# Kernel optimization log

Hardware: AMD Instinct MI355X
Metric: run time of the kernel (lower is better)

The kernel has to match this reference:

```python
import jax, jax.numpy as jnp
import numpy as np

VOCAB = 100000
EMBED = 64
HIDDEN = 256
SEQ = 200
BATCH = 4096


def setup_inputs() -> dict:
    key = jax.random.key(0)
    ks = jax.random.split(key, 12)
    s = 0.02
    return {
        "user_hist": jax.random.randint(ks[0], (BATCH, SEQ), 0, VOCAB),
        "target_item": jax.random.randint(ks[1], (BATCH,), 0, VOCAB),
        "user_emb": jax.random.normal(ks[2], (VOCAB, EMBED), jnp.float32) * s,
        "item_emb": jax.random.normal(ks[3], (VOCAB, EMBED), jnp.float32) * s,
        "attn_w1": jax.random.normal(ks[4], (4 * EMBED, HIDDEN), jnp.float32) * s,
        "attn_b1": jnp.zeros((HIDDEN,), jnp.float32),
        "attn_w2": jax.random.normal(ks[5], (HIDDEN, 1), jnp.float32) * s,
        "attn_b2": jnp.zeros((1,), jnp.float32),
        "mlp_w1": jax.random.normal(ks[6], (2 * EMBED, HIDDEN), jnp.float32) * s,
        "mlp_b1": jnp.zeros((HIDDEN,), jnp.float32),
        "mlp_w2": jax.random.normal(ks[7], (HIDDEN, 1), jnp.float32) * s,
        "mlp_b2": jnp.zeros((1,), jnp.float32),
    }


def reference(user_hist, target_item, user_emb, item_emb,
              attn_w1, attn_b1, attn_w2, attn_b2,
              mlp_w1, mlp_b1, mlp_w2, mlp_b2):
    # [B, S, E] history embeddings, [B, 1, E] target embedding
    h = user_emb[user_hist]
    t = item_emb[target_item][:, None, :]
    tb = jnp.broadcast_to(t, h.shape)
    # attention MLP over [B, S, 4E]
    att_in = jnp.concatenate([h, tb, h - t, h * t], axis=-1)
    att_h = jax.nn.relu(att_in @ attn_w1 + attn_b1)
    att_logits = (att_h @ attn_w2 + attn_b2)[..., 0]            # [B, S]
    att_w = jax.nn.softmax(att_logits, axis=-1)[..., None]      # [B, S, 1]
    user_interest = jnp.sum(h * att_w, axis=1)                  # [B, E]
    # prediction head on [B, 2E]
    mlp_in = jnp.concatenate([user_interest, t[:, 0, :]], axis=-1)
    mlp_h = jax.nn.relu(mlp_in @ mlp_w1 + mlp_b1)
    out = jax.nn.sigmoid(mlp_h @ mlp_w2 + mlp_b2)               # [B, 1]
    return out
```

## Files before the change

### kernel.cpp

```cpp
#include <hip/hip_runtime.h>
#include <math.h>

#define EMBED   64
#define HIDDEN  256
#define SEQ     200
#define SEQP    208
#define MT      13

typedef _Float16 f16x8  __attribute__((ext_vector_type(8)));
typedef _Float16 half2_t __attribute__((ext_vector_type(2)));
typedef float    f32x4  __attribute__((ext_vector_type(4)));

__device__ inline float fdot2(half2_t a, half2_t b, float c) {
  return __builtin_amdgcn_fdot2(a, b, c, false);
}

__global__ void din_precompute(const float* __restrict__ attn_w1,
                               const float* __restrict__ mlp_w1,
                               _Float16* __restrict__ fragB,
                               _Float16* __restrict__ D2f,
                               _Float16* __restrict__ fragB2) {
  const int gid = blockIdx.x * 256 + threadIdx.x;
  if (gid < 4096) {
    const int nt = gid >> 8, kc = (gid >> 6) & 3, lane = gid & 63;
    const int n = nt * 16 + (lane & 15);
    const int kbase = kc * 32 + (lane >> 4) * 8;
    #pragma unroll
    for (int j = 0; j < 8; ++j) {
      const int k = kbase + j;
      float v;
      if (k < 64) v = attn_w1[k * HIDDEN + n] + attn_w1[(128 + k) * HIDDEN + n];
      else        v = attn_w1[(192 + (k - 64)) * HIDDEN + n];
      fragB[gid * 8 + j] = (_Float16)v;
    }
  } else if (gid < 8192) {
    const int f = (gid - 4096) * 4;
    #pragma unroll
    for (int i = 0; i < 4; ++i) {
      const int idx = f + i;
      const int kk = idx & 7, t2 = idx >> 3;
      const int j = t2 & 255, c = t2 >> 8;
      const int k = c * 8 + kk;
      D2f[idx] = (_Float16)(attn_w1[(64 + k) * HIDDEN + j] - attn_w1[(128 + k) * HIDDEN + j]);
    }
  } else {
    const int g = gid - 8192;
    const int nt = g >> 8, kc = (g >> 6) & 3, lane = g & 63;
    const int n = nt * 16 + (lane & 15);
    const int kbase = kc * 32 + (lane >> 4) * 8;
    #pragma unroll
    for (int j = 0; j < 8; ++j)
      fragB2[g * 8 + j] = (_Float16)mlp_w1[(kbase + j) * HIDDEN + n];
  }
}

__global__ __launch_bounds__(256, 3)
void din_fused_kernel(const int* __restrict__ user_hist,
                      const int* __restrict__ target_item,
                      const float* __restrict__ user_emb,
                      const float* __restrict__ item_emb,
                      const float* __restrict__ attn_b1,
                      const float* __restrict__ attn_w2,
                      const float* __restrict__ mlp_b1,
                      const float* __restrict__ mlp_w2,
                      const float* __restrict__ mlp_b2,
                      const _Float16* __restrict__ fragB,
                      const _Float16* __restrict__ D2f,
                      const _Float16* __restrict__ fragB2,
                      float* __restrict__ out)
{
  __shared__ __align__(16) _Float16 Hf[MT * 2 * 64 * 8];
  __shared__ __align__(16) _Float16 t16[EMBED];
  __shared__ float cl[HIDDEN];
  __shared__ float w2s[HIDDEN];
  __shared__ float b1h[HIDDEN];
  __shared__ float w2h[HIDDEN];
  __shared__ float lp[4][SEQP];
  __shared__ float weights[SEQP];
  __shared__ __align__(16) _Float16 mi16[EMBED];
  __shared__ float red[8];

  const int b    = blockIdx.x;
  const int tid  = threadIdx.x;
  const int lane = tid & 63;
  const int wave = tid >> 6;
  const int m    = lane & 15;
  const int quad = lane >> 4;

  if (tid < EMBED) t16[tid] = (_Float16)item_emb[target_item[b] * EMBED + tid];
  w2s[tid] = attn_w2[tid];
  b1h[tid] = mlp_b1[tid];
  w2h[tid] = mlp_w2[tid];
  __syncthreads();

  {
    const int* hist = user_hist + b * SEQ;
    for (int slot = tid; slot < MT * 2 * 64; slot += 256) {
      const int ln = slot & 63, kcomb = slot >> 6;
      const int st = kcomb >> 1, kc = kcomb & 1;
      const int s = st * 16 + (ln & 15);
      const int kb = kc * 32 + (ln >> 4) * 8;
      f16x8 v;
      if (s < SEQ) {
        const float4* src = reinterpret_cast<const float4*>(&user_emb[hist[s] * EMBED + kb]);
        const float4 x = src[0], y = src[1];
        v = f16x8{(_Float16)x.x, (_Float16)x.y, (_Float16)x.z, (_Float16)x.w,
                  (_Float16)y.x, (_Float16)y.y, (_Float16)y.z, (_Float16)y.w};
      } else {
        v = f16x8{(_Float16)0.f, (_Float16)0.f, (_Float16)0.f, (_Float16)0.f,
                  (_Float16)0.f, (_Float16)0.f, (_Float16)0.f, (_Float16)0.f};
      }
      *reinterpret_cast<f16x8*>(&Hf[slot * 8]) = v;
    }
  }

  {
    float cj = attn_b1[tid];
    const f16x8* dp = reinterpret_cast<const f16x8*>(D2f);
    #pragma unroll
    for (int c = 0; c < 8; ++c) {
      const f16x8 dv = dp[c * HIDDEN + tid];
      const f16x8 tv = *reinterpret_cast<const f16x8*>(&t16[c * 8]);
      const half2_t* d2 = reinterpret_cast<const half2_t*>(&dv);
      const half2_t* t2 = reinterpret_cast<const half2_t*>(&tv);
      cj = fdot2(d2[0], t2[0], cj);
      cj = fdot2(d2[1], t2[1], cj);
      cj = fdot2(d2[2], t2[2], cj);
      cj = fdot2(d2[3], t2[3], cj);
    }
    cl[tid] = cj;
  }
  __syncthreads();

  f16x8 Aw[4][4];
  #pragma unroll
  for (int i = 0; i < 4; ++i)
    #pragma unroll
    for (int kc = 0; kc < 4; ++kc)
      Aw[i][kc] = reinterpret_cast<const f16x8*>(fragB)[((4 * wave + i) * 4 + kc) * 64 + lane];

  const f16x8 tv0 = *reinterpret_cast<const f16x8*>(&t16[quad * 8]);
  const f16x8 tv1 = *reinterpret_cast<const f16x8*>(&t16[32 + quad * 8]);

  float cn[4][4], w2n[4][4];
  #pragma unroll
  for (int i = 0; i < 4; ++i)
    #pragma unroll
    for (int r = 0; r < 4; ++r) {
      const int n = (4 * wave + i) * 16 + quad * 4 + r;
      cn[i][r]  = cl[n];
      w2n[i][r] = w2s[n];
    }

  for (int st = 0; st < MT; ++st) {
    const f16x8 bh0 = *reinterpret_cast<const f16x8*>(&Hf[((st * 2 + 0) * 64 + lane) * 8]);
    const f16x8 bh1 = *reinterpret_cast<const f16x8*>(&Hf[((st * 2 + 1) * 64 + lane) * 8]);
    const f16x8 bh2 = bh0 * tv0;
    const f16x8 bh3 = bh1 * tv1;
    float lg = 0.f;
    #pragma unroll
    for (int i = 0; i < 4; ++i) {
      f32x4 acc = {cn[i][0], cn[i][1], cn[i][2], cn[i][3]};
      acc = __builtin_amdgcn_mfma_f32_16x16x32_f16(Aw[i][0], bh0, acc, 0, 0, 0);
      acc = __builtin_amdgcn_mfma_f32_16x16x32_f16(Aw[i][1], bh1, acc, 0, 0, 0);
      acc = __builtin_amdgcn_mfma_f32_16x16x32_f16(Aw[i][2], bh2, acc, 0, 0, 0);
      acc = __builtin_amdgcn_mfma_f32_16x16x32_f16(Aw[i][3], bh3, acc, 0, 0, 0);
      #pragma unroll
      for (int r = 0; r < 4; ++r)
        lg += fmaxf(acc[r], 0.0f) * w2n[i][r];
    }
    lg += __shfl_xor(lg, 16, 64);
    lg += __shfl_xor(lg, 32, 64);
    if (lane < 16) lp[wave][st * 16 + lane] = lg;
  }
  __syncthreads();

  float v = -INFINITY;
  if (tid < SEQ) v = lp[0][tid] + lp[1][tid] + lp[2][tid] + lp[3][tid];
  float mx = v;
  #pragma unroll
  for (int off = 32; off; off >>= 1) mx = fmaxf(mx, __shfl_xor(mx, off, 64));
  if (lane == 0) red[wave] = mx;
  __syncthreads();
  mx = fmaxf(fmaxf(red[0], red[1]), fmaxf(red[2], red[3]));
  float e = (tid < SEQ) ? expf(v - mx) : 0.0f;
  float ssum = e;
  #pragma unroll
  for (int off = 32; off; off >>= 1) ssum += __shfl_xor(ssum, off, 64);
  if (lane == 0) red[4 + wave] = ssum;
  __syncthreads();
  const float tot = red[4] + red[5] + red[6] + red[7];
  if (tid < SEQP) weights[tid] = (tid < SEQ) ? e / tot : 0.0f;
  __syncthreads();

  {
    float pk[16];
    #pragma unroll
    for (int i = 0; i < 16; ++i) pk[i] = 0.f;
    for (int st = wave; st < MT; st += 4) {
      const f16x8 bh0 = *reinterpret_cast<const f16x8*>(&Hf[((st * 2 + 0) * 64 + lane) * 8]);
      const f16x8 bh1 = *reinterpret_cast<const f16x8*>(&Hf[((st * 2 + 1) * 64 + lane) * 8]);
      const float wt = weights[st * 16 + m];
      #pragma unroll
      for (int j = 0; j < 8; ++j) {
        pk[j]     += wt * (float)bh0[j];
        pk[8 + j] += wt * (float)bh1[j];
      }
    }
    #pragma unroll
    for (int i = 0; i < 16; ++i) {
      float p = pk[i];
      p += __shfl_xor(p, 1, 64);
      p += __shfl_xor(p, 2, 64);
      p += __shfl_xor(p, 4, 64);
      p += __shfl_xor(p, 8, 64);
      pk[i] = p;
    }
    if (m == 0) {
      #pragma unroll
      for (int i = 0; i < 16; ++i) {
        const int k = (i >> 3) * 32 + quad * 8 + (i & 7);
        lp[wave][k] = pk[i];
      }
    }
  }
  __syncthreads();
  if (tid < EMBED)
    mi16[tid] = (_Float16)(lp[0][tid] + lp[1][tid] + lp[2][tid] + lp[3][tid]);
  __syncthreads();

  {
    f16x8 A2[4][4];
    #pragma unroll
    for (int i = 0; i < 4; ++i)
      #pragma unroll
      for (int kc = 0; kc < 4; ++kc)
        A2[i][kc] = reinterpret_cast<const f16x8*>(fragB2)[((4 * wave + i) * 4 + kc) * 64 + lane];
    const f16x8 mb0 = *reinterpret_cast<const f16x8*>(&mi16[quad * 8]);
    const f16x8 mb1 = *reinterpret_cast<const f16x8*>(&mi16[32 + quad * 8]);
    float z = 0.f;
    #pragma unroll
    for (int i = 0; i < 4; ++i) {
      float bb[4], ww[4];
      #pragma unroll
      for (int r = 0; r < 4; ++r) {
        const int n = (4 * wave + i) * 16 + quad * 4 + r;
        bb[r] = b1h[n];
        ww[r] = w2h[n];
      }
      f32x4 acc = {bb[0], bb[1], bb[2], bb[3]};
      acc = __builtin_amdgcn_mfma_f32_16x16x32_f16(A2[i][0], mb0, acc, 0, 0, 0);
      acc = __builtin_amdgcn_mfma_f32_16x16x32_f16(A2[i][1], mb1, acc, 0, 0, 0);
      acc = __builtin_amdgcn_mfma_f32_16x16x32_f16(A2[i][2], tv0, acc, 0, 0, 0);
      acc = __builtin_amdgcn_mfma_f32_16x16x32_f16(A2[i][3], tv1, acc, 0, 0, 0);
      #pragma unroll
      for (int r = 0; r < 4; ++r)
        z += fmaxf(acc[r], 0.0f) * ww[r];
    }
    z += __shfl_xor(z, 16, 64);
    z += __shfl_xor(z, 32, 64);
    if (lane == 0) red[wave] = z;
  }
  __syncthreads();
  if (tid == 0) {
    const float zz = red[0] + red[1] + red[2] + red[3] + mlp_b2[0];
    out[b] = 1.0f / (1.0f + expf(-zz));
  }
}

extern "C" void kernel_launch(void* const* d_in, const int* in_sizes, int n_in,
                              void* d_out, int out_size, void* d_ws, size_t ws_size,
                              hipStream_t stream) {
  const int*   user_hist   = (const int*)  d_in[0];
  const int*   target_item = (const int*)  d_in[1];
  const float* user_emb    = (const float*)d_in[2];
  const float* item_emb    = (const float*)d_in[3];
  const float* attn_w1     = (const float*)d_in[4];
  const float* attn_b1     = (const float*)d_in[5];
  const float* attn_w2     = (const float*)d_in[6];
  const float* mlp_w1      = (const float*)d_in[8];
  const float* mlp_b1      = (const float*)d_in[9];
  const float* mlp_w2      = (const float*)d_in[10];
  const float* mlp_b2      = (const float*)d_in[11];
  float* out = (float*)d_out;

  _Float16* fragB  = (_Float16*)d_ws;
  _Float16* D2f    = (_Float16*)((char*)d_ws + 65536);
  _Float16* fragB2 = (_Float16*)((char*)d_ws + 98304);

  din_precompute<<<48, 256, 0, stream>>>(attn_w1, mlp_w1, fragB, D2f, fragB2);

  const int batch = in_sizes[1];
  din_fused_kernel<<<batch, 256, 0, stream>>>(
      user_hist, target_item, user_emb, item_emb,
      attn_b1, attn_w2, mlp_b1, mlp_w2, mlp_b2,
      fragB, D2f, fragB2, out);
}
```

Measured before the change: 206.1 us.

## Switch attention MLP to FP8 MFMA with scaled operands and 512-thread blocks

Converts the gathered history embeddings and the attention weight fragments to FP8 (scaled by 16 to stay in range) and uses fp8 MFMA. The target-dependent h*t term is folded into per-block FP8 weights (W3*t), so the hidden GEMM needs only the history operand. This halves LDS footprint and MFMA operand bytes. Blocks also grow to 8 waves of 512 threads, each wave owning two hidden tiles, to raise occupancy and shrink per-thread register state. The cost is FP8 accuracy loss in both the attention logits and the weighted sum, which now reads the FP8 history copy.

```diff
diff --git a/kernel.cpp b/kernel.cpp
--- a/kernel.cpp
+++ b/kernel.cpp
@@ -10,6 +10,7 @@
 typedef _Float16 f16x8  __attribute__((ext_vector_type(8)));
 typedef _Float16 half2_t __attribute__((ext_vector_type(2)));
 typedef float    f32x4  __attribute__((ext_vector_type(4)));
+typedef float    f32x2  __attribute__((ext_vector_type(2)));
 
 __device__ inline float fdot2(half2_t a, half2_t b, float c) {
   return __builtin_amdgcn_fdot2(a, b, c, false);
@@ -17,22 +18,32 @@
 
 __global__ void din_precompute(const float* __restrict__ attn_w1,
                                const float* __restrict__ mlp_w1,
-                               _Float16* __restrict__ fragB,
+                               uint2* __restrict__ fragB8,
+                               _Float16* __restrict__ fragW3,
                                _Float16* __restrict__ D2f,
                                _Float16* __restrict__ fragB2) {
   const int gid = blockIdx.x * 256 + threadIdx.x;
-  if (gid < 4096) {
-    const int nt = gid >> 8, kc = (gid >> 6) & 3, lane = gid & 63;
-    const int n = nt * 16 + (lane & 15);
-    const int kbase = kc * 32 + (lane >> 4) * 8;
-    #pragma unroll
-    for (int j = 0; j < 8; ++j) {
-      const int k = kbase + j;
-      float v;
-      if (k < 64) v = attn_w1[k * HIDDEN + n] + attn_w1[(128 + k) * HIDDEN + n];
-      else        v = attn_w1[(192 + (k - 64)) * HIDDEN + n];
-      fragB[gid * 8 + j] = (_Float16)v;
-    }
+  if (gid < 2048) {
+    const int i = gid >> 7, rem = gid & 127, kc = rem >> 6, lane = rem & 63;
+    const int n = i * 16 + (lane & 15);
+    const int kb = kc * 32 + (lane >> 4) * 8;
+    float v[8];
+    #pragma unroll
+    for (int j = 0; j < 8; ++j)
+      v[j] = 16.0f * (attn_w1[(kb + j) * HIDDEN + n] + attn_w1[(128 + kb + j) * HIDDEN + n]);
+    int lo = __builtin_amdgcn_cvt_pk_fp8_f32(v[0], v[1], 0, false);
+    lo     = __builtin_amdgcn_cvt_pk_fp8_f32(v[2], v[3], lo, true);
+    int hi = __builtin_amdgcn_cvt_pk_fp8_f32(v[4], v[5], 0, false);
+    hi     = __builtin_amdgcn_cvt_pk_fp8_f32(v[6], v[7], hi, true);
+    fragB8[gid] = uint2{(unsigned)lo, (unsigned)hi};
+  } else if (gid < 4096) {
+    const int g = gid - 2048;
+    const int i = g >> 7, rem = g & 127, kc = rem >> 6, lane = rem & 63;
+    const int n = i * 16 + (lane & 15);
+    const int kb = kc * 32 + (lane >> 4) * 8;
+    #pragma unroll
+    for (int j = 0; j < 8; ++j)
+      fragW3[g * 8 + j] = (_Float16)(16.0f * attn_w1[(192 + kb + j) * HIDDEN + n]);
   } else if (gid < 8192) {
     const int f = (gid - 4096) * 4;
     #pragma unroll
@@ -47,14 +58,14 @@
     const int g = gid - 8192;
     const int nt = g >> 8, kc = (g >> 6) & 3, lane = g & 63;
     const int n = nt * 16 + (lane & 15);
-    const int kbase = kc * 32 + (lane >> 4) * 8;
+    const int kb = kc * 32 + (lane >> 4) * 8;
     #pragma unroll
     for (int j = 0; j < 8; ++j)
-      fragB2[g * 8 + j] = (_Float16)mlp_w1[(kbase + j) * HIDDEN + n];
+      fragB2[g * 8 + j] = (_Float16)mlp_w1[(kb + j) * HIDDEN + n];
   }
 }
 
-__global__ __launch_bounds__(256, 3)
+__global__ __launch_bounds__(512, 8)
 void din_fused_kernel(const int* __restrict__ user_hist,
                       const int* __restrict__ target_item,
                       const float* __restrict__ user_emb,
@@ -64,21 +75,19 @@
                       const float* __restrict__ mlp_b1,
                       const float* __restrict__ mlp_w2,
                       const float* __restrict__ mlp_b2,
-                      const _Float16* __restrict__ fragB,
+                      const uint2* __restrict__ fragB8,
+                      const _Float16* __restrict__ fragW3,
                       const _Float16* __restrict__ D2f,
                       const _Float16* __restrict__ fragB2,
                       float* __restrict__ out)
 {
-  __shared__ __align__(16) _Float16 Hf[MT * 2 * 64 * 8];
+  __shared__ __align__(16) uint2 Hf8[MT * 2 * 64];
   __shared__ __align__(16) _Float16 t16[EMBED];
   __shared__ float cl[HIDDEN];
-  __shared__ float w2s[HIDDEN];
-  __shared__ float b1h[HIDDEN];
-  __shared__ float w2h[HIDDEN];
-  __shared__ float lp[4][SEQP];
+  __shared__ float lp[8][SEQP];
   __shared__ float weights[SEQP];
   __shared__ __align__(16) _Float16 mi16[EMBED];
-  __shared__ float red[8];
+  __shared__ float red[16];
 
   const int b    = blockIdx.x;
   const int tid  = threadIdx.x;
@@ -88,33 +97,37 @@
   const int quad = lane >> 4;
 
   if (tid < EMBED) t16[tid] = (_Float16)item_emb[target_item[b] * EMBED + tid];
-  w2s[tid] = attn_w2[tid];
-  b1h[tid] = mlp_b1[tid];
-  w2h[tid] = mlp_w2[tid];
-  __syncthreads();
+
+  long long Aw8[2][2];
+  #pragma unroll
+  for (int i = 0; i < 2; ++i)
+    #pragma unroll
+    for (int c = 0; c < 2; ++c)
+      Aw8[i][c] = __builtin_bit_cast(long long, fragB8[((2 * wave + i) * 2 + c) * 64 + lane]);
 
   {
     const int* hist = user_hist + b * SEQ;
-    for (int slot = tid; slot < MT * 2 * 64; slot += 256) {
+    for (int slot = tid; slot < MT * 2 * 64; slot += 512) {
       const int ln = slot & 63, kcomb = slot >> 6;
       const int st = kcomb >> 1, kc = kcomb & 1;
       const int s = st * 16 + (ln & 15);
       const int kb = kc * 32 + (ln >> 4) * 8;
-      f16x8 v;
+      uint2 pv = uint2{0u, 0u};
       if (s < SEQ) {
         const float4* src = reinterpret_cast<const float4*>(&user_emb[hist[s] * EMBED + kb]);
         const float4 x = src[0], y = src[1];
-        v = f16x8{(_Float16)x.x, (_Float16)x.y, (_Float16)x.z, (_Float16)x.w,
-                  (_Float16)y.x, (_Float16)y.y, (_Float16)y.z, (_Float16)y.w};
-      } else {
-        v = f16x8{(_Float16)0.f, (_Float16)0.f, (_Float16)0.f, (_Float16)0.f,
-                  (_Float16)0.f, (_Float16)0.f, (_Float16)0.f, (_Float16)0.f};
+        int lo = __builtin_amdgcn_cvt_pk_fp8_f32(16.f * x.x, 16.f * x.y, 0, false);
+        lo     = __builtin_amdgcn_cvt_pk_fp8_f32(16.f * x.z, 16.f * x.w, lo, true);
+        int hi = __builtin_amdgcn_cvt_pk_fp8_f32(16.f * y.x, 16.f * y.y, 0, false);
+        hi     = __builtin_amdgcn_cvt_pk_fp8_f32(16.f * y.z, 16.f * y.w, hi, true);
+        pv = uint2{(unsigned)lo, (unsigned)hi};
       }
-      *reinterpret_cast<f16x8*>(&Hf[slot * 8]) = v;
-    }
-  }
-
-  {
+      Hf8[slot] = pv;
+    }
+  }
+  __syncthreads();
+
+  if (tid < HIDDEN) {
     float cj = attn_b1[tid];
     const f16x8* dp = reinterpret_cast<const f16x8*>(D2f);
     #pragma unroll
@@ -130,41 +143,44 @@
     }
     cl[tid] = cj;
   }
-  __syncthreads();
-
-  f16x8 Aw[4][4];
-  #pragma unroll
-  for (int i = 0; i < 4; ++i)
-    #pragma unroll
-    for (int kc = 0; kc < 4; ++kc)
-      Aw[i][kc] = reinterpret_cast<const f16x8*>(fragB)[((4 * wave + i) * 4 + kc) * 64 + lane];
-
-  const f16x8 tv0 = *reinterpret_cast<const f16x8*>(&t16[quad * 8]);
-  const f16x8 tv1 = *reinterpret_cast<const f16x8*>(&t16[32 + quad * 8]);
-
-  float cn[4][4], w2n[4][4];
-  #pragma unroll
-  for (int i = 0; i < 4; ++i)
+
+  long long AwT[2][2];
+  #pragma unroll
+  for (int i = 0; i < 2; ++i)
+    #pragma unroll
+    for (int c = 0; c < 2; ++c) {
+      const f16x8 w3v = reinterpret_cast<const f16x8*>(fragW3)[((2 * wave + i) * 2 + c) * 64 + lane];
+      const f16x8 tw  = *reinterpret_cast<const f16x8*>(&t16[c * 32 + quad * 8]);
+      const f16x8 p = w3v * tw;
+      int lo = __builtin_amdgcn_cvt_pk_fp8_f32((float)p[0], (float)p[1], 0, false);
+      lo     = __builtin_amdgcn_cvt_pk_fp8_f32((float)p[2], (float)p[3], lo, true);
+      int hi = __builtin_amdgcn_cvt_pk_fp8_f32((float)p[4], (float)p[5], 0, false);
+      hi     = __builtin_amdgcn_cvt_pk_fp8_f32((float)p[6], (float)p[7], hi, true);
+      AwT[i][c] = __builtin_bit_cast(long long, uint2{(unsigned)lo, (unsigned)hi});
+    }
+  __syncthreads();
+
+  float cn[2][4], w2n[2][4];
+  #pragma unroll
+  for (int i = 0; i < 2; ++i)
     #pragma unroll
     for (int r = 0; r < 4; ++r) {
-      const int n = (4 * wave + i) * 16 + quad * 4 + r;
-      cn[i][r]  = cl[n];
-      w2n[i][r] = w2s[n];
+      const int n = (2 * wave + i) * 16 + quad * 4 + r;
+      cn[i][r]  = 256.0f * cl[n];
+      w2n[i][r] = attn_w2[n] * (1.0f / 256.0f);
     }
 
   for (int st = 0; st < MT; ++st) {
-    const f16x8 bh0 = *reinterpret_cast<const f16x8*>(&Hf[((st * 2 + 0) * 64 + lane) * 8]);
-    const f16x8 bh1 = *reinterpret_cast<const f16x8*>(&Hf[((st * 2 + 1) * 64 + lane) * 8]);
-    const f16x8 bh2 = bh0 * tv0;
-    const f16x8 bh3 = bh1 * tv1;
+    const long long b0 = __builtin_bit_cast(long long, Hf8[(st * 2 + 0) * 64 + lane]);
+    const long long b1 = __builtin_bit_cast(long long, Hf8[(st * 2 + 1) * 64 + lane]);
     float lg = 0.f;
     #pragma unroll
-    for (int i = 0; i < 4; ++i) {
+    for (int i = 0; i < 2; ++i) {
       f32x4 acc = {cn[i][0], cn[i][1], cn[i][2], cn[i][3]};
-      acc = __builtin_amdgcn_mfma_f32_16x16x32_f16(Aw[i][0], bh0, acc, 0, 0, 0);
-      acc = __builtin_amdgcn_mfma_f32_16x16x32_f16(Aw[i][1], bh1, acc, 0, 0, 0);
-      acc = __builtin_amdgcn_mfma_f32_16x16x32_f16(Aw[i][2], bh2, acc, 0, 0, 0);
-      acc = __builtin_amdgcn_mfma_f32_16x16x32_f16(Aw[i][3], bh3, acc, 0, 0, 0);
+      acc = __builtin_amdgcn_mfma_f32_16x16x32_fp8_fp8(Aw8[i][0], b0, acc, 0, 0, 0);
+      acc = __builtin_amdgcn_mfma_f32_16x16x32_fp8_fp8(Aw8[i][1], b1, acc, 0, 0, 0);
+      acc = __builtin_amdgcn_mfma_f32_16x16x32_fp8_fp8(AwT[i][0], b0, acc, 0, 0, 0);
+      acc = __builtin_amdgcn_mfma_f32_16x16x32_fp8_fp8(AwT[i][1], b1, acc, 0, 0, 0);
       #pragma unroll
       for (int r = 0; r < 4; ++r)
         lg += fmaxf(acc[r], 0.0f) * w2n[i][r];
@@ -176,83 +192,85 @@
   __syncthreads();
 
   float v = -INFINITY;
-  if (tid < SEQ) v = lp[0][tid] + lp[1][tid] + lp[2][tid] + lp[3][tid];
+  if (tid < SEQ)
+    v = lp[0][tid] + lp[1][tid] + lp[2][tid] + lp[3][tid]
+      + lp[4][tid] + lp[5][tid] + lp[6][tid] + lp[7][tid];
   float mx = v;
   #pragma unroll
   for (int off = 32; off; off >>= 1) mx = fmaxf(mx, __shfl_xor(mx, off, 64));
   if (lane == 0) red[wave] = mx;
   __syncthreads();
-  mx = fmaxf(fmaxf(red[0], red[1]), fmaxf(red[2], red[3]));
+  mx = fmaxf(fmaxf(fmaxf(red[0], red[1]), fmaxf(red[2], red[3])),
+             fmaxf(fmaxf(red[4], red[5]), fmaxf(red[6], red[7])));
   float e = (tid < SEQ) ? expf(v - mx) : 0.0f;
   float ssum = e;
   #pragma unroll
   for (int off = 32; off; off >>= 1) ssum += __shfl_xor(ssum, off, 64);
-  if (lane == 0) red[4 + wave] = ssum;
-  __syncthreads();
-  const float tot = red[4] + red[5] + red[6] + red[7];
+  if (lane == 0) red[8 + wave] = ssum;
+  __syncthreads();
+  const float tot = red[8] + red[9] + red[10] + red[11]
+                  + red[12] + red[13] + red[14] + red[15];
   if (tid < SEQP) weights[tid] = (tid < SEQ) ? e / tot : 0.0f;
   __syncthreads();
 
   {
-    float pk[16];
-    #pragma unroll
-    for (int i = 0; i < 16; ++i) pk[i] = 0.f;
-    for (int st = wave; st < MT; st += 4) {
-      const f16x8 bh0 = *reinterpret_cast<const f16x8*>(&Hf[((st * 2 + 0) * 64 + lane) * 8]);
-      const f16x8 bh1 = *reinterpret_cast<const f16x8*>(&Hf[((st * 2 + 1) * 64 + lane) * 8]);
+    const int kc = wave & 1, g = wave >> 1;
+    float pk[8];
+    #pragma unroll
+    for (int j = 0; j < 8; ++j) pk[j] = 0.f;
+    for (int st = g; st < MT; st += 4) {
       const float wt = weights[st * 16 + m];
-      #pragma unroll
-      for (int j = 0; j < 8; ++j) {
-        pk[j]     += wt * (float)bh0[j];
-        pk[8 + j] += wt * (float)bh1[j];
-      }
-    }
-    #pragma unroll
-    for (int i = 0; i < 16; ++i) {
-      float p = pk[i];
+      const uint2 hv = Hf8[(st * 2 + kc) * 64 + lane];
+      const f32x2 f0 = __builtin_amdgcn_cvt_pk_f32_fp8((int)hv.x, false);
+      const f32x2 f1 = __builtin_amdgcn_cvt_pk_f32_fp8((int)hv.x, true);
+      const f32x2 f2 = __builtin_amdgcn_cvt_pk_f32_fp8((int)hv.y, false);
+      const f32x2 f3 = __builtin_amdgcn_cvt_pk_f32_fp8((int)hv.y, true);
+      pk[0] += wt * f0.x;  pk[1] += wt * f0.y;
+      pk[2] += wt * f1.x;  pk[3] += wt * f1.y;
+      pk[4] += wt * f2.x;  pk[5] += wt * f2.y;
+      pk[6] += wt * f3.x;  pk[7] += wt * f3.y;
+    }
+    #pragma unroll
+    for (int j = 0; j < 8; ++j) {
+      float p = pk[j];
       p += __shfl_xor(p, 1, 64);
       p += __shfl_xor(p, 2, 64);
       p += __shfl_xor(p, 4, 64);
       p += __shfl_xor(p, 8, 64);
-      pk[i] = p;
+      pk[j] = p;
     }
     if (m == 0) {
       #pragma unroll
-      for (int i = 0; i < 16; ++i) {
-        const int k = (i >> 3) * 32 + quad * 8 + (i & 7);
-        lp[wave][k] = pk[i];
-      }
+      for (int j = 0; j < 8; ++j)
+        lp[g][kc * 32 + quad * 8 + j] = pk[j];
     }
   }
   __syncthreads();
   if (tid < EMBED)
-    mi16[tid] = (_Float16)(lp[0][tid] + lp[1][tid] + lp[2][tid] + lp[3][tid]);
+    mi16[tid] = (_Float16)((lp[0][tid] + lp[1][tid] + lp[2][tid] + lp[3][tid]) * 0.0625f);
   __syncthreads();
 
   {
-    f16x8 A2[4][4];
-    #pragma unroll
-    for (int i = 0; i < 4; ++i)
-      #pragma unroll
-      for (int kc = 0; kc < 4; ++kc)
-        A2[i][kc] = reinterpret_cast<const f16x8*>(fragB2)[((4 * wave + i) * 4 + kc) * 64 + lane];
     const f16x8 mb0 = *reinterpret_cast<const f16x8*>(&mi16[quad * 8]);
     const f16x8 mb1 = *reinterpret_cast<const f16x8*>(&mi16[32 + quad * 8]);
+    const f16x8 tv0 = *reinterpret_cast<const f16x8*>(&t16[quad * 8]);
+    const f16x8 tv1 = *reinterpret_cast<const f16x8*>(&t16[32 + quad * 8]);
     float z = 0.f;
     #pragma unroll
-    for (int i = 0; i < 4; ++i) {
+    for (int i = 0; i < 2; ++i) {
+      const f16x8* B2 = reinterpret_cast<const f16x8*>(fragB2) + ((2 * wave + i) * 4) * 64 + lane;
       float bb[4], ww[4];
       #pragma unroll
       for (int r = 0; r < 4; ++r) {
-        const int n = (4 * wave + i) * 16 + quad * 4 + r;
-        bb[r] = b1h[n];
-        ww[r] = w2h[n];
+        const int n = (2 * wave + i) * 16 + quad * 4 + r;
+        bb[r] = mlp_b1[n];
+        ww[r] = mlp_w2[n];
       }
       f32x4 acc = {bb[0], bb[1], bb[2], bb[3]};
-      acc = __builtin_amdgcn_mfma_f32_16x16x32_f16(A2[i][0], mb0, acc, 0, 0, 0);
-      acc = __builtin_amdgcn_mfma_f32_16x16x32_f16(A2[i][1], mb1, acc, 0, 0, 0);
-      acc = __builtin_amdgcn_mfma_f32_16x16x32_f16(A2[i][2], tv0, acc, 0, 0, 0);
-      acc = __builtin_amdgcn_mfma_f32_16x16x32_f16(A2[i][3], tv1, acc, 0, 0, 0);
+      acc = __builtin_amdgcn_mfma_f32_16x16x32_f16(B2[0],       mb0, acc, 0, 0, 0);
+      acc = __builtin_amdgcn_mfma_f32_16x16x32_f16(B2[64],      mb1, acc, 0, 0, 0);
+      acc = __builtin_amdgcn_mfma_f32_16x16x32_f16(B2[128],     tv0, acc, 0, 0, 0);
+      acc = __builtin_amdgcn_mfma_f32_16x16x32_f16(B2[192],     tv1, acc, 0, 0, 0);
       #pragma unroll
       for (int r = 0; r < 4; ++r)
         z += fmaxf(acc[r], 0.0f) * ww[r];
@@ -263,7 +281,8 @@
   }
   __syncthreads();
   if (tid == 0) {
-    const float zz = red[0] + red[1] + red[2] + red[3] + mlp_b2[0];
+    const float zz = red[0] + red[1] + red[2] + red[3]
+                   + red[4] + red[5] + red[6] + red[7] + mlp_b2[0];
     out[b] = 1.0f / (1.0f + expf(-zz));
   }
 }
@@ -284,15 +303,16 @@
   const float* mlp_b2      = (const float*)d_in[11];
   float* out = (float*)d_out;
 
-  _Float16* fragB  = (_Float16*)d_ws;
-  _Float16* D2f    = (_Float16*)((char*)d_ws + 65536);
-  _Float16* fragB2 = (_Float16*)((char*)d_ws + 98304);
-
-  din_precompute<<<48, 256, 0, stream>>>(attn_w1, mlp_w1, fragB, D2f, fragB2);
+  uint2*    fragB8 = (uint2*)d_ws;
+  _Float16* fragW3 = (_Float16*)((char*)d_ws + 16384);
+  _Float16* D2f    = (_Float16*)((char*)d_ws + 49152);
+  _Float16* fragB2 = (_Float16*)((char*)d_ws + 81920);
+
+  din_precompute<<<48, 256, 0, stream>>>(attn_w1, mlp_w1, fragB8, fragW3, D2f, fragB2);
 
   const int batch = in_sizes[1];
-  din_fused_kernel<<<batch, 256, 0, stream>>>(
+  din_fused_kernel<<<batch, 512, 0, stream>>>(
       user_hist, target_item, user_emb, item_emb,
       attn_b1, attn_w2, mlp_b1, mlp_w2, mlp_b2,
-      fragB, D2f, fragB2, out);
+      fragB8, fragW3, D2f, fragB2, out);
 }
```

Result: faster. 183.1 us (-11.2%).
